# Optimization experiments

Hardware: AMD Instinct MI355X
Metric: run time of the kernel (lower is better)

Reference implementation:

```python
import jax, jax.numpy as jnp
import numpy as np
import math

D_K = 64
ROUNDS = 4
BUCKET_LEN = 64


def _l2norm(x, axis):
    n = jnp.sqrt(jnp.sum(x * x, axis=axis, keepdims=True))
    return x / jnp.maximum(n, 1e-12)


def _look_back(x):
    # x: (B, n_buckets, bucket_len, ...) -> (B, n_buckets, 2*bucket_len, ...)
    # each bucket is concatenated with the previous bucket (wrapping at 0)
    shift = jnp.concatenate([x[:, -1:], x[:, :-1]], axis=1)
    return jnp.concatenate([shift, x], axis=2)


def _lsh_hash(query, rand_matrix):
    # returns position-tagged hashes: bucket_id * L + position, shape (B, L, R)
    B, L, D = query.shape
    qn = _l2norm(query, -1)
    rm = _l2norm(rand_matrix, 1)  # normalize over d_k dim, as in torch code
    xR = jnp.einsum('bld,bdrn->blrn', qn, rm)
    h = jnp.argmax(jnp.concatenate([xR, -xR], axis=-1), axis=-1).astype(jnp.int32)
    return h * L + jnp.arange(L, dtype=jnp.int32)[None, :, None]


def _attend(query, value, hash_indice, original_indice, sorted_hashes):
    B, L, D = query.shape
    nb = L // BUCKET_LEN
    R = ROUNDS
    # gather queries into hash-sorted order, per round: (B, L, D, R)
    rq = jnp.take_along_axis(query[:, :, :, None], hash_indice[:, :, None, :], axis=1)
    rq = rq.reshape(B, nb, BUCKET_LEN, D, R)
    lk = _l2norm(_look_back(rq), -2)  # keys = normalized lookback queries (shared QK)
    qk = jnp.einsum('bnijk,bnljk->bnilk', rq, lk) / math.sqrt(D_K)  # (B,nb,bl,2bl,R)
    # mask cross-bucket pairs
    sh = (sorted_hashes // L).reshape(B, nb, BUCKET_LEN, R)
    qk = jnp.where(sh[..., None, :] != _look_back(sh)[..., None, :, :], -1e9, qk)
    # mask self-attention (causal=False so no causal mask)
    qi = hash_indice.reshape(B, nb, BUCKET_LEN, R).astype(jnp.int32)
    ki = _look_back(qi)
    qk = jnp.where(qi[..., None, :] == ki[..., None, :, :], -1e5, qk)
    qk = qk.reshape(B, L, 2 * BUCKET_LEN, R)
    lse = jax.scipy.special.logsumexp(qk, axis=2)  # (B, L, R)
    p = jnp.exp(qk - lse[:, :, None, :]).reshape(B, nb, BUCKET_LEN, 2 * BUCKET_LEN, R)
    # gather values into sorted order and apply lookback attention
    rv = jnp.take_along_axis(value[:, :, :, None], hash_indice[:, :, None, :], axis=1)
    rv = rv.reshape(B, nb, BUCKET_LEN, D, R)
    att = jnp.einsum('bnijl,bnjkl->bnikl', p, _look_back(rv)).reshape(B, L, D, R)
    # scatter back to original order
    att = jnp.take_along_axis(att, original_indice[:, :, None, :], axis=1)
    lse = jnp.take_along_axis(lse, original_indice, axis=1)
    # NOTE: faithful to source, softmax over dim=1 (sequence dim)
    w = jax.nn.softmax(lse, axis=1)  # (B, L, R)
    return jnp.einsum('blir,blr->bli', att, w)  # (B, L, D)


def setup_inputs() -> dict:
    key = jax.random.key(0)
    k1, k2, k3 = jax.random.split(key, 3)
    B, L, D = 16, 8192, D_K
    n_buckets = L // BUCKET_LEN
    return {
        'query': jax.random.normal(k1, (B, L, D), jnp.float32),
        'value': jax.random.normal(k2, (B, L, D), jnp.float32),
        'rand_matrix': jax.random.normal(k3, (B, D, ROUNDS, n_buckets // 2), jnp.float32),
    }


def reference(query, value, rand_matrix):
    hashes = _lsh_hash(query, rand_matrix)          # (B, L, R) int32
    hash_indice = jnp.argsort(hashes, axis=1)       # sort positions by hash
    sorted_hashes = jnp.take_along_axis(hashes, hash_indice, axis=1)
    original_indice = jnp.argsort(hash_indice, axis=1)  # inverse permutation
    return _attend(query, value, hash_indice.astype(jnp.int32),
                   original_indice.astype(jnp.int32), sorted_hashes)
```

## Files before the change

kernel.cpp:

```cpp
#include <hip/hip_runtime.h>
#include <math.h>

#define B_   16
#define L_   8192
#define D_   64
#define R_   4
#define NB_  128
#define NH_  64

typedef float v2f __attribute__((ext_vector_type(2)));

__device__ __forceinline__ float dpp_xor1(float x) {
    return __int_as_float(__builtin_amdgcn_mov_dpp(__float_as_int(x), 0xB1, 0xf, 0xf, true));
}
__device__ __forceinline__ float dpp_xor2(float x) {
    return __int_as_float(__builtin_amdgcn_mov_dpp(__float_as_int(x), 0x4E, 0xf, 0xf, true));
}
__device__ __forceinline__ float quad_bcast0(float x) {
    return __int_as_float(__builtin_amdgcn_mov_dpp(__float_as_int(x), 0x00, 0xf, 0xf, true));
}
__device__ __forceinline__ float quad_bcast1(float x) {
    return __int_as_float(__builtin_amdgcn_mov_dpp(__float_as_int(x), 0x55, 0xf, 0xf, true));
}
__device__ __forceinline__ float quad_bcast2(float x) {
    return __int_as_float(__builtin_amdgcn_mov_dpp(__float_as_int(x), 0xAA, 0xf, 0xf, true));
}
__device__ __forceinline__ float quad_bcast3(float x) {
    return __int_as_float(__builtin_amdgcn_mov_dpp(__float_as_int(x), 0xFF, 0xf, 0xf, true));
}

__global__ __launch_bounds__(64) void k_rmnorm(const float* __restrict__ rm, double* __restrict__ rmn) {
    int b = blockIdx.x >> 2, r = blockIdx.x & 3;
    int n = threadIdx.x;
    float v[D_];
    double ss = 0.0;
    #pragma unroll
    for (int d = 0; d < D_; ++d) {
        float f = rm[((size_t)(b * D_ + d) * R_ + r) * NH_ + n];
        v[d] = f;
        ss += (double)f * (double)f;
    }
    double nrm = sqrt(ss); if (nrm < 1e-12) nrm = 1e-12;
    double inv = 1.0 / nrm;
    double* o = rmn + ((size_t)(b * R_ + r) * NH_ + n) * D_;
    #pragma unroll
    for (int d = 0; d < D_; ++d) o[d] = (double)v[d] * inv;
}

__global__ __launch_bounds__(256) void k_hash(const float* __restrict__ q, const double* __restrict__ rmn,
                                              float* __restrict__ rn, int* __restrict__ h) {
    __shared__ float rms[NH_ * D_];
    int b = blockIdx.z, r = blockIdx.y;
    int l = blockIdx.x * 256 + threadIdx.x;
    const double* src = rmn + (size_t)(b * R_ + r) * NH_ * D_;
    for (int i = threadIdx.x; i < NH_ * D_; i += 256) rms[i] = (float)src[i];
    const float* qp = q + ((size_t)b * L_ + l) * D_;
    v2f qv2[D_ / 2];
    double ss = 0.0;
    #pragma unroll
    for (int d = 0; d < D_; d += 4) {
        float4 f = *(const float4*)(qp + d);
        qv2[d >> 1]       = (v2f){f.x, f.y};
        qv2[(d >> 1) + 1] = (v2f){f.z, f.w};
        ss += (double)f.x * f.x + (double)f.y * f.y + (double)f.z * f.z + (double)f.w * f.w;
    }
    __syncthreads();
    float best = -1.0e30f, second = -1.0e30f; int bi = 0;
    for (int n = 0; n < NH_; ++n) {
        const float* kp = &rms[n * D_];
        v2f a0 = (v2f){0.f, 0.f}, a1 = a0;
        #pragma unroll
        for (int d = 0; d < D_; d += 4) {
            float4 kk = *(const float4*)(kp + d);
            a0 = __builtin_elementwise_fma(qv2[d >> 1],       (v2f){kk.x, kk.y}, a0);
            a1 = __builtin_elementwise_fma(qv2[(d >> 1) + 1], (v2f){kk.z, kk.w}, a1);
        }
        float s = (a0.x + a0.y) + (a1.x + a1.y);
        if (s > best)       { second = best; best = s; bi = n; }
        else if (s > second)  second = s;
        float ns = -s;
        if (ns > best)      { second = best; best = ns; bi = n + NH_; }
        else if (ns > second) second = ns;
    }
    float qn = (float)sqrt(ss);
    if (best - second < 1.2e-5f * qn + 1.0e-7f) {
        double bestd = -1.0e300; bi = 0;
        for (int n = 0; n < NH_; ++n) {
            const double* kp = src + n * D_;
            double a0 = 0, a1 = 0, a2 = 0, a3 = 0;
            #pragma unroll
            for (int d = 0; d < D_; d += 4) {
                a0 = fma((double)qv2[d >> 1].x,       kp[d],     a0);
                a1 = fma((double)qv2[d >> 1].y,       kp[d + 1], a1);
                a2 = fma((double)qv2[(d >> 1) + 1].x, kp[d + 2], a2);
                a3 = fma((double)qv2[(d >> 1) + 1].y, kp[d + 3], a3);
            }
            double s = (a0 + a1) + (a2 + a3);
            if (s > bestd)  { bestd = s;  bi = n; }
            if (-s > bestd) { bestd = -s; bi = n + NH_; }
        }
    }
    h[(size_t)(b * R_ + r) * L_ + l] = bi;
    if (r == 0) {
        double nrm = sqrt(ss); if (nrm < 1e-12) nrm = 1e-12;
        rn[(size_t)b * L_ + l] = (float)(1.0 / nrm);
    }
}

__global__ __launch_bounds__(256) void k_sort(const int* __restrict__ h, const float* __restrict__ rn,
                                              int* __restrict__ iv, int2* __restrict__ rec) {
    __shared__ unsigned int cnt[NB_ * 257];
    __shared__ unsigned int wsum[4];
    int br = blockIdx.x;
    const int* hh = h + (size_t)br * L_;
    const float* rnb = rn + (size_t)(br >> 2) * L_;
    int t = threadIdx.x;
    for (int i = t; i < NB_ * 257; i += 256) cnt[i] = 0;
    __syncthreads();
    int base = t * 32;
    for (int i = 0; i < 32; ++i) { int bk = hh[base + i]; cnt[bk * 257 + t]++; }
    __syncthreads();
    int fb = t * 128;
    unsigned int local = 0;
    for (int i = 0; i < 128; ++i) { unsigned g = fb + i; local += cnt[g + (g >> 8)]; }
    unsigned int v = local;
    #pragma unroll
    for (int off = 1; off < 64; off <<= 1) {
        unsigned int u = __shfl_up(v, off);
        if ((t & 63) >= off) v += u;
    }
    if ((t & 63) == 63) wsum[t >> 6] = v;
    __syncthreads();
    unsigned int wbase = 0;
    for (int w = 0; w < (t >> 6); ++w) wbase += wsum[w];
    unsigned int run = wbase + v - local;
    for (int i = 0; i < 128; ++i) {
        unsigned g = fb + i;
        unsigned int c0 = cnt[g + (g >> 8)];
        cnt[g + (g >> 8)] = run; run += c0;
    }
    __syncthreads();
    int* ivp = iv + (size_t)br * L_;
    int2* rp = rec + (size_t)br * L_;
    for (int i = 0; i < 32; ++i) {
        int l = base + i; int bk = hh[l];
        unsigned int pos = cnt[bk * 257 + t]++;
        ivp[l] = (int)pos;
        rp[pos] = make_int2(l | (bk << 16), __float_as_int(rnb[l]));
    }
}

__global__ __launch_bounds__(128, 2) void k_flash(const float* __restrict__ q, const float* __restrict__ val,
                                                  const int2* __restrict__ rec, float* __restrict__ lse,
                                                  const float* __restrict__ gm, const float* __restrict__ gs,
                                                  float* __restrict__ out, float* __restrict__ contrib,
                                                  int r_fixed, int omode) {
    __shared__ float kt[2][16 * 80];
    __shared__ float vt[2][16 * 80];
    __shared__ int2  krc[2][16];
    int w   = threadIdx.x >> 6;
    int tid = threadIdx.x & 63;
    int c = blockIdx.x * 2 + w, b = blockIdx.z;
    int r = (r_fixed < 0) ? (int)blockIdx.y : r_fixed;
    size_t sbase = (size_t)(b * R_ + r) * L_;
    const int2* recs = rec + sbase;
    const float* qb = q   + (size_t)b * L_ * D_;
    const float* vb = val + (size_t)b * L_ * D_;
    int loadv = (omode != 2);
    int h = tid & 3;
    int posq = c * 64 + (tid >> 2) * 4;
    int2 rown = recs[posq + h];
    int own_w0 = rown.x;
    int own_bk = own_w0 & 0xFFFF0000;
    float m_own = 0.125f / __int_as_float(rown.y);
    int minbk = __builtin_amdgcn_readfirstlane(recs[c * 64].x) & 0xFFFF0000;
    int maxbk = __builtin_amdgcn_readfirstlane(recs[c * 64 + 63].x) & 0xFFFF0000;
    int mls[4];
    #pragma unroll
    for (int qq = 0; qq < 4; ++qq) mls[qq] = recs[posq + qq].x & 0xFFFF;
    int ownpos = posq + h;
    v2f qv2[4][8];
    #pragma unroll
    for (int qq = 0; qq < 4; ++qq) {
        const float* qp = qb + (size_t)mls[qq] * D_ + h * 16;
        #pragma unroll
        for (int i = 0; i < 16; i += 4) {
            float4 f = *(const float4*)(qp + i);
            qv2[qq][i >> 1]       = (v2f){f.x, f.y};
            qv2[qq][(i >> 1) + 1] = (v2f){f.z, f.w};
        }
    }
    float ps[4] = {0.0f, 0.0f, 0.0f, 0.0f};
    v2f acc2[4][8];
    #pragma unroll
    for (int qq = 0; qq < 4; ++qq)
        #pragma unroll
        for (int i = 0; i < 8; ++i) acc2[qq][i] = (v2f){0.0f, 0.0f};

    #pragma unroll 1
    for (int s = 0; s < 8; ++s) {
        int ck = ((c + NB_ - 1 + (s >> 2)) & (NB_ - 1)) * 64 + (s & 3) * 16;
        int sfir = __builtin_amdgcn_readfirstlane(recs[ck].x) & 0xFFFF0000;
        int slas = __builtin_amdgcn_readfirstlane(recs[ck + 15].x) & 0xFFFF0000;
        if (slas < minbk || sfir > maxbk) continue;
        {
            int rw = tid >> 2, cc = tid & 3;
            int kl = recs[ck + rw].x & 0xFFFF;
            const float* kp = qb + (size_t)kl * D_ + cc * 16;
            float* kd = &kt[w][rw * 80 + cc * 20];
            #pragma unroll
            for (int i = 0; i < 16; i += 4) *(float4*)(kd + i) = *(const float4*)(kp + i);
            if (loadv) {
                const float* vp = vb + (size_t)kl * D_ + cc * 16;
                float* vd = &vt[w][rw * 80 + cc * 20];
                #pragma unroll
                for (int i = 0; i < 16; i += 4) *(float4*)(vd + i) = *(const float4*)(vp + i);
            }
            if (tid < 16) krc[w][tid] = recs[ck + tid];
        }
        #pragma unroll
        for (int j = 0; j < 16; ++j) {
            int2 kv = krc[w][j];
            int bkj = __builtin_amdgcn_readfirstlane(kv.x) & 0xFFFF0000;
            if (bkj < minbk || bkj > maxbk) continue;
            const float* kpj = &kt[w][j * 80 + h * 20];
            v2f a0 = (v2f){0.f, 0.f}, a1 = a0, a2 = a0, a3 = a0;
            #pragma unroll
            for (int i = 0; i < 16; i += 4) {
                float4 kk = *(const float4*)(kpj + i);
                v2f kA = (v2f){kk.x, kk.y}, kB = (v2f){kk.z, kk.w};
                int i2 = i >> 1;
                a0 = __builtin_elementwise_fma(qv2[0][i2], kA, a0);
                a0 = __builtin_elementwise_fma(qv2[0][i2 + 1], kB, a0);
                a1 = __builtin_elementwise_fma(qv2[1][i2], kA, a1);
                a1 = __builtin_elementwise_fma(qv2[1][i2 + 1], kB, a1);
                a2 = __builtin_elementwise_fma(qv2[2][i2], kA, a2);
                a2 = __builtin_elementwise_fma(qv2[2][i2 + 1], kB, a2);
                a3 = __builtin_elementwise_fma(qv2[3][i2], kA, a3);
                a3 = __builtin_elementwise_fma(qv2[3][i2 + 1], kB, a3);
            }
            float p0 = a0.x + a0.y, p1 = a1.x + a1.y, p2 = a2.x + a2.y, p3 = a3.x + a3.y;
            bool b0 = (h & 1), b1 = (h & 2) != 0;
            float u0 = b0 ? p1 : p0;
            float t0 = b0 ? p0 : p1;
            u0 += dpp_xor1(t0);
            float u2 = b0 ? p3 : p2;
            float t2 = b0 ? p2 : p3;
            u2 += dpp_xor1(t2);
            float dot = b1 ? u2 : u0;
            float t3 = b1 ? u0 : u2;
            dot += dpp_xor2(t3);
            float skr = __int_as_float(kv.y) * 0.125f;
            float sc = dot * skr;
            sc = (own_bk == (kv.x & 0xFFFF0000)) ? sc : -1.0e9f;
            if (own_w0 == kv.x) sc = -1.0e5f;
            float p = __expf(sc - m_own);
            ps[j & 3] += p;
            if (loadv) {
                v2f P0 = (v2f){quad_bcast0(p), quad_bcast0(p)};
                v2f P1 = (v2f){quad_bcast1(p), quad_bcast1(p)};
                v2f P2 = (v2f){quad_bcast2(p), quad_bcast2(p)};
                v2f P3 = (v2f){quad_bcast3(p), quad_bcast3(p)};
                const float* vpj = &vt[w][j * 80 + h * 20];
                float4 vv0 = *(const float4*)(vpj + 0);
                float4 vv1 = *(const float4*)(vpj + 4);
                float4 vv2 = *(const float4*)(vpj + 8);
                float4 vv3 = *(const float4*)(vpj + 12);
                v2f vAa = (v2f){vv0.x, vv0.y}, vAb = (v2f){vv0.z, vv0.w};
                v2f vAc = (v2f){vv1.x, vv1.y}, vAd = (v2f){vv1.z, vv1.w};
                v2f vAe = (v2f){vv2.x, vv2.y}, vAf = (v2f){vv2.z, vv2.w};
                v2f vAg = (v2f){vv3.x, vv3.y}, vAh = (v2f){vv3.z, vv3.w};
                acc2[0][0] = __builtin_elementwise_fma(P0, vAa, acc2[0][0]);
                acc2[0][1] = __builtin_elementwise_fma(P0, vAb, acc2[0][1]);
                acc2[0][2] = __builtin_elementwise_fma(P0, vAc, acc2[0][2]);
                acc2[0][3] = __builtin_elementwise_fma(P0, vAd, acc2[0][3]);
                acc2[0][4] = __builtin_elementwise_fma(P0, vAe, acc2[0][4]);
                acc2[0][5] = __builtin_elementwise_fma(P0, vAf, acc2[0][5]);
                acc2[0][6] = __builtin_elementwise_fma(P0, vAg, acc2[0][6]);
                acc2[0][7] = __builtin_elementwise_fma(P0, vAh, acc2[0][7]);
                acc2[1][0] = __builtin_elementwise_fma(P1, vAa, acc2[1][0]);
                acc2[1][1] = __builtin_elementwise_fma(P1, vAb, acc2[1][1]);
                acc2[1][2] = __builtin_elementwise_fma(P1, vAc, acc2[1][2]);
                acc2[1][3] = __builtin_elementwise_fma(P1, vAd, acc2[1][3]);
                acc2[1][4] = __builtin_elementwise_fma(P1, vAe, acc2[1][4]);
                acc2[1][5] = __builtin_elementwise_fma(P1, vAf, acc2[1][5]);
                acc2[1][6] = __builtin_elementwise_fma(P1, vAg, acc2[1][6]);
                acc2[1][7] = __builtin_elementwise_fma(P1, vAh, acc2[1][7]);
                acc2[2][0] = __builtin_elementwise_fma(P2, vAa, acc2[2][0]);
                acc2[2][1] = __builtin_elementwise_fma(P2, vAb, acc2[2][1]);
                acc2[2][2] = __builtin_elementwise_fma(P2, vAc, acc2[2][2]);
                acc2[2][3] = __builtin_elementwise_fma(P2, vAd, acc2[2][3]);
                acc2[2][4] = __builtin_elementwise_fma(P2, vAe, acc2[2][4]);
                acc2[2][5] = __builtin_elementwise_fma(P2, vAf, acc2[2][5]);
                acc2[2][6] = __builtin_elementwise_fma(P2, vAg, acc2[2][6]);
                acc2[2][7] = __builtin_elementwise_fma(P2, vAh, acc2[2][7]);
                acc2[3][0] = __builtin_elementwise_fma(P3, vAa, acc2[3][0]);
                acc2[3][1] = __builtin_elementwise_fma(P3, vAb, acc2[3][1]);
                acc2[3][2] = __builtin_elementwise_fma(P3, vAc, acc2[3][2]);
                acc2[3][3] = __builtin_elementwise_fma(P3, vAd, acc2[3][3]);
                acc2[3][4] = __builtin_elementwise_fma(P3, vAe, acc2[3][4]);
                acc2[3][5] = __builtin_elementwise_fma(P3, vAf, acc2[3][5]);
                acc2[3][6] = __builtin_elementwise_fma(P3, vAg, acc2[3][6]);
                acc2[3][7] = __builtin_elementwise_fma(P3, vAh, acc2[3][7]);
            }
        }
    }
    float sum = (ps[0] + ps[1]) + (ps[2] + ps[3]);
    float lse_own, inv_own;
    if (sum > 0.0f) { lse_own = m_own + logf(sum); inv_own = 1.0f / sum; }
    else            { lse_own = -3.0e38f;          inv_own = 0.0f; }
    if (omode != 3) lse[sbase + ownpos] = lse_own;
    if (omode == 0 || omode == 1) {
        float ivs[4];
        ivs[0] = quad_bcast0(inv_own); ivs[1] = quad_bcast1(inv_own);
        ivs[2] = quad_bcast2(inv_own); ivs[3] = quad_bcast3(inv_own);
        float* cbase = contrib + ((omode == 0) ? (size_t)(b * R_ + r) * L_ : (size_t)b * L_) * D_;
        #pragma unroll
        for (int qq = 0; qq < 4; ++qq) {
            float* cp = cbase + (size_t)(posq + qq) * D_ + h * 16;
            #pragma unroll
            for (int i = 0; i < 16; i += 4) {
                int i2 = i >> 1;
                float4 o;
                o.x = acc2[qq][i2].x * ivs[qq];     o.y = acc2[qq][i2].y * ivs[qq];
                o.z = acc2[qq][i2 + 1].x * ivs[qq]; o.w = acc2[qq][i2 + 1].y * ivs[qq];
                *(float4*)(cp + i) = o;
            }
        }
    } else if (omode == 3) {
        int brr = b * R_ + r;
        float gmv = gm[brr], gsv = gs[brr];
        float ls4[4], iv4[4];
        ls4[0] = quad_bcast0(lse_own); ls4[1] = quad_bcast1(lse_own);
        ls4[2] = quad_bcast2(lse_own); ls4[3] = quad_bcast3(lse_own);
        iv4[0] = quad_bcast0(inv_own); iv4[1] = quad_bcast1(inv_own);
        iv4[2] = quad_bcast2(inv_own); iv4[3] = quad_bcast3(inv_own);
        #pragma unroll
        for (int qq = 0; qq < 4; ++qq) {
            float wq = __expf(ls4[qq] - gmv) * gsv * iv4[qq];
            float* op = out + ((size_t)b * L_ + mls[qq]) * D_ + h * 16;
            #pragma unroll
            for (int i = 0; i < 8; ++i) {
                unsafeAtomicAdd(op + 2 * i,     wq * acc2[qq][i].x);
                unsafeAtomicAdd(op + 2 * i + 1, wq * acc2[qq][i].y);
            }
        }
    }
}

__global__ __launch_bounds__(256) void k_wred(const float* __restrict__ lse, float* __restrict__ gm,
                                              float* __restrict__ gs, int r_w) {
    __shared__ float  sm[4];
    __shared__ double sd[4];
    int br = (r_w < 0) ? (int)blockIdx.x : ((int)blockIdx.x * R_ + r_w);
    const float* x = lse + (size_t)br * L_;
    int t = threadIdx.x;
    float mx = -3.0e38f;
    for (int i = t; i < L_; i += 256) mx = fmaxf(mx, x[i]);
    #pragma unroll
    for (int o = 32; o; o >>= 1) mx = fmaxf(mx, __shfl_down(mx, o));
    if ((t & 63) == 0) sm[t >> 6] = mx;
    __syncthreads();
    mx = fmaxf(fmaxf(sm[0], sm[1]), fmaxf(sm[2], sm[3]));
    double s = 0.0;
    for (int i = t; i < L_; i += 256) s += exp((double)x[i] - (double)mx);
    #pragma unroll
    for (int o = 32; o; o >>= 1) s += __shfl_down(s, o);
    if ((t & 63) == 0) sd[t >> 6] = s;
    __syncthreads();
    if (t == 0) { gm[br] = mx; gs[br] = (float)(1.0 / (sd[0] + sd[1] + sd[2] + sd[3])); }
}

__global__ __launch_bounds__(256) void k_comb_full(const float* __restrict__ contrib,
                                                   const int* __restrict__ iv,
                                                   const float* __restrict__ lse,
                                                   const float* __restrict__ gm,
                                                   const float* __restrict__ gs,
                                                   float* __restrict__ out) {
    int gid = blockIdx.x * 256 + threadIdx.x;
    int row = gid >> 2;
    int ch  = (gid & 3) * 16;
    int b = row >> 13, l = row & (L_ - 1);
    float s[16];
    #pragma unroll
    for (int i = 0; i < 16; ++i) s[i] = 0.0f;
    #pragma unroll
    for (int r = 0; r < R_; ++r) {
        int brr = b * R_ + r;
        int pos = iv[(size_t)brr * L_ + l];
        float w = expf(lse[(size_t)brr * L_ + pos] - gm[brr]) * gs[brr];
        const float* cp = contrib + ((size_t)brr * L_ + pos) * D_ + ch;
        #pragma unroll
        for (int i = 0; i < 16; i += 4) {
            float4 f = *(const float4*)(cp + i);
            s[i]   = fmaf(w, f.x, s[i]);   s[i+1] = fmaf(w, f.y, s[i+1]);
            s[i+2] = fmaf(w, f.z, s[i+2]); s[i+3] = fmaf(w, f.w, s[i+3]);
        }
    }
    float* op = out + (size_t)row * D_ + ch;
    #pragma unroll
    for (int i = 0; i < 16; i += 4) {
        float4 o; o.x = s[i]; o.y = s[i+1]; o.z = s[i+2]; o.w = s[i+3];
        *(float4*)(op + i) = o;
    }
}

__global__ __launch_bounds__(256) void k_comb_add(const float* __restrict__ contrib,
                                                  const int* __restrict__ iv,
                                                  const float* __restrict__ lse,
                                                  const float* __restrict__ gm,
                                                  const float* __restrict__ gs,
                                                  float* __restrict__ out, int r) {
    int gid = blockIdx.x * 256 + threadIdx.x;
    int row = gid >> 2;
    int ch  = (gid & 3) * 16;
    int b = row >> 13, l = row & (L_ - 1);
    int brr = b * R_ + r;
    int pos = iv[(size_t)brr * L_ + l];
    float w = expf(lse[(size_t)brr * L_ + pos] - gm[brr]) * gs[brr];
    const float* cp = contrib + ((size_t)b * L_ + pos) * D_ + ch;
    float* op = out + (size_t)row * D_ + ch;
    #pragma unroll
    for (int i = 0; i < 16; i += 4) {
        float4 f = *(const float4*)(cp + i);
        float4 o = *(const float4*)(op + i);
        o.x = fmaf(w, f.x, o.x); o.y = fmaf(w, f.y, o.y);
        o.z = fmaf(w, f.z, o.z); o.w = fmaf(w, f.w, o.w);
        *(float4*)(op + i) = o;
    }
}

#define OFF_RMN     0u
#define OFF_REC     0u
#define OFF_RN      4194304u
#define OFF_H       4718592u
#define OFF_LSE     6815744u
#define OFF_GM      8912896u
#define OFF_GS      8913152u
#define OFF_INV     8913408u
#define OFF_CONTRIB 11010560u
#define CONTRIB_FULL_BYTES  134217728ull
#define CONTRIB_SLICE_BYTES 33554432ull

extern "C" void kernel_launch(void* const* d_in, const int* in_sizes, int n_in,
                              void* d_out, int out_size, void* d_ws, size_t ws_size,
                              hipStream_t stream) {
    const float* q  = (const float*)d_in[0];
    const float* v  = (const float*)d_in[1];
    const float* rm = (const float*)d_in[2];
    float* out = (float*)d_out;
    char* ws = (char*)d_ws;
    double* rmn = (double*)(ws + OFF_RMN);
    int2*   rec = (int2*)(ws + OFF_REC);
    float*  rn  = (float*)(ws + OFF_RN);
    int*    h   = (int*)(ws + OFF_H);
    float*  lse = (float*)(ws + OFF_LSE);
    float*  gm  = (float*)(ws + OFF_GM);
    float*  gs  = (float*)(ws + OFF_GS);
    int*    iv  = (int*)(ws + OFF_INV);
    float*  contrib = (float*)(ws + OFF_CONTRIB);

    int tierA = (ws_size >= (size_t)OFF_CONTRIB + CONTRIB_FULL_BYTES) ? 1 : 0;
    int tierB = (!tierA && ws_size >= (size_t)OFF_CONTRIB + CONTRIB_SLICE_BYTES) ? 1 : 0;

    hipLaunchKernelGGL(k_rmnorm, dim3(B_ * R_), dim3(64), 0, stream, rm, rmn);
    hipLaunchKernelGGL(k_hash, dim3(L_ / 256, R_, B_), dim3(256), 0, stream, q, rmn, rn, h);
    hipLaunchKernelGGL(k_sort, dim3(B_ * R_), dim3(256), 0, stream, h, rn, iv, rec);

    if (tierA) {
        hipLaunchKernelGGL(k_flash, dim3(NB_ / 2, R_, B_), dim3(128), 0, stream, q, v, rec,
                           lse, gm, gs, out, contrib, -1, 0);
        hipLaunchKernelGGL(k_wred, dim3(B_ * R_), dim3(256), 0, stream, lse, gm, gs, -1);
        hipLaunchKernelGGL(k_comb_full, dim3(B_ * L_ * 4 / 256), dim3(256), 0, stream,
                           contrib, iv, lse, gm, gs, out);
    } else if (tierB) {
        hipMemsetAsync(d_out, 0, (size_t)B_ * L_ * D_ * sizeof(float), stream);
        for (int r = 0; r < R_; ++r) {
            hipLaunchKernelGGL(k_flash, dim3(NB_ / 2, 1, B_), dim3(128), 0, stream, q, v, rec,
                               lse, gm, gs, out, contrib, r, 1);
            hipLaunchKernelGGL(k_wred, dim3(B_), dim3(256), 0, stream, lse, gm, gs, r);
            hipLaunchKernelGGL(k_comb_add, dim3(B_ * L_ * 4 / 256), dim3(256), 0, stream,
                               contrib, iv, lse, gm, gs, out, r);
        }
    } else {
        hipMemsetAsync(d_out, 0, (size_t)B_ * L_ * D_ * sizeof(float), stream);
        hipLaunchKernelGGL(k_flash, dim3(NB_ / 2, R_, B_), dim3(128), 0, stream, q, v, rec,
                           lse, gm, gs, out, contrib, -1, 2);
        hipLaunchKernelGGL(k_wred, dim3(B_ * R_), dim3(256), 0, stream, lse, gm, gs, -1);
        hipLaunchKernelGGL(k_flash, dim3(NB_ / 2, R_, B_), dim3(128), 0, stream, q, v, rec,
                           lse, gm, gs, out, contrib, -1, 3);
    }
}
```

Before: 530.1 us.

## Hash two positions per thread, prestore float rotations, skip out-of-range key loads

The hash kernel now computes two sequence positions per thread, so each shared-memory read of the rotation matrix feeds twice as many FMAs, and the grid is halved to match. The normalisation kernel also writes a float copy of the rotations, so the hash kernel loads it with float4 instead of converting doubles. In the flash kernel, key and value rows whose bucket falls outside the query tile's range are no longer loaded into shared memory. The float copy shares its workspace offset with the inverse-permutation buffer, which is safe only if that buffer is written after hashing. Doubling per-thread work also raises register pressure.

After: 560.4 us. 5.7% more time.

```diff
diff --git a/kernel.cpp b/kernel.cpp
--- a/kernel.cpp
+++ b/kernel.cpp
@@ -29,7 +29,8 @@
     return __int_as_float(__builtin_amdgcn_mov_dpp(__float_as_int(x), 0xFF, 0xf, 0xf, true));
 }
 
-__global__ __launch_bounds__(64) void k_rmnorm(const float* __restrict__ rm, double* __restrict__ rmn) {
+__global__ __launch_bounds__(64) void k_rmnorm(const float* __restrict__ rm, double* __restrict__ rmn,
+                                               float* __restrict__ rmf) {
     int b = blockIdx.x >> 2, r = blockIdx.x & 3;
     int n = threadIdx.x;
     float v[D_];
@@ -42,68 +43,115 @@
     }
     double nrm = sqrt(ss); if (nrm < 1e-12) nrm = 1e-12;
     double inv = 1.0 / nrm;
-    double* o = rmn + ((size_t)(b * R_ + r) * NH_ + n) * D_;
-    #pragma unroll
-    for (int d = 0; d < D_; ++d) o[d] = (double)v[d] * inv;
-}
-
-__global__ __launch_bounds__(256) void k_hash(const float* __restrict__ q, const double* __restrict__ rmn,
-                                              float* __restrict__ rn, int* __restrict__ h) {
+    double* o  = rmn + ((size_t)(b * R_ + r) * NH_ + n) * D_;
+    float*  of = rmf + ((size_t)(b * R_ + r) * NH_ + n) * D_;
+    #pragma unroll
+    for (int d = 0; d < D_; ++d) {
+        double dv = (double)v[d] * inv;
+        o[d] = dv;
+        of[d] = (float)dv;
+    }
+}
+
+__global__ __launch_bounds__(256, 2) void k_hash(const float* __restrict__ q, const double* __restrict__ rmn,
+                                                 const float* __restrict__ rmf,
+                                                 float* __restrict__ rn, int* __restrict__ h) {
     __shared__ float rms[NH_ * D_];
     int b = blockIdx.z, r = blockIdx.y;
-    int l = blockIdx.x * 256 + threadIdx.x;
+    int t = threadIdx.x;
+    int l0 = blockIdx.x * 512 + t;
+    int l1 = l0 + 256;
     const double* src = rmn + (size_t)(b * R_ + r) * NH_ * D_;
-    for (int i = threadIdx.x; i < NH_ * D_; i += 256) rms[i] = (float)src[i];
-    const float* qp = q + ((size_t)b * L_ + l) * D_;
-    v2f qv2[D_ / 2];
-    double ss = 0.0;
+    const float* srcf = rmf + (size_t)(b * R_ + r) * NH_ * D_;
+    for (int i = t * 4; i < NH_ * D_; i += 1024)
+        *(float4*)&rms[i] = *(const float4*)&srcf[i];
+    const float* qp0 = q + ((size_t)b * L_ + l0) * D_;
+    const float* qp1 = q + ((size_t)b * L_ + l1) * D_;
+    v2f qa[D_ / 2], qb[D_ / 2];
+    double ssa = 0.0, ssb = 0.0;
     #pragma unroll
     for (int d = 0; d < D_; d += 4) {
-        float4 f = *(const float4*)(qp + d);
-        qv2[d >> 1]       = (v2f){f.x, f.y};
-        qv2[(d >> 1) + 1] = (v2f){f.z, f.w};
-        ss += (double)f.x * f.x + (double)f.y * f.y + (double)f.z * f.z + (double)f.w * f.w;
-    }
-    __syncthreads();
-    float best = -1.0e30f, second = -1.0e30f; int bi = 0;
+        float4 f = *(const float4*)(qp0 + d);
+        qa[d >> 1]       = (v2f){f.x, f.y};
+        qa[(d >> 1) + 1] = (v2f){f.z, f.w};
+        ssa += (double)f.x * f.x + (double)f.y * f.y + (double)f.z * f.z + (double)f.w * f.w;
+        float4 g = *(const float4*)(qp1 + d);
+        qb[d >> 1]       = (v2f){g.x, g.y};
+        qb[(d >> 1) + 1] = (v2f){g.z, g.w};
+        ssb += (double)g.x * g.x + (double)g.y * g.y + (double)g.z * g.z + (double)g.w * g.w;
+    }
+    __syncthreads();
+    float besta = -1.0e30f, seconda = -1.0e30f; int bia = 0;
+    float bestb = -1.0e30f, secondb = -1.0e30f; int bib = 0;
     for (int n = 0; n < NH_; ++n) {
         const float* kp = &rms[n * D_];
-        v2f a0 = (v2f){0.f, 0.f}, a1 = a0;
+        v2f a0 = (v2f){0.f, 0.f}, a1 = a0, c0 = a0, c1 = a0;
         #pragma unroll
         for (int d = 0; d < D_; d += 4) {
             float4 kk = *(const float4*)(kp + d);
-            a0 = __builtin_elementwise_fma(qv2[d >> 1],       (v2f){kk.x, kk.y}, a0);
-            a1 = __builtin_elementwise_fma(qv2[(d >> 1) + 1], (v2f){kk.z, kk.w}, a1);
-        }
-        float s = (a0.x + a0.y) + (a1.x + a1.y);
-        if (s > best)       { second = best; best = s; bi = n; }
-        else if (s > second)  second = s;
-        float ns = -s;
-        if (ns > best)      { second = best; best = ns; bi = n + NH_; }
-        else if (ns > second) second = ns;
-    }
-    float qn = (float)sqrt(ss);
-    if (best - second < 1.2e-5f * qn + 1.0e-7f) {
-        double bestd = -1.0e300; bi = 0;
+            v2f kA = (v2f){kk.x, kk.y}, kB = (v2f){kk.z, kk.w};
+            int i2 = d >> 1;
+            a0 = __builtin_elementwise_fma(qa[i2],     kA, a0);
+            a1 = __builtin_elementwise_fma(qa[i2 + 1], kB, a1);
+            c0 = __builtin_elementwise_fma(qb[i2],     kA, c0);
+            c1 = __builtin_elementwise_fma(qb[i2 + 1], kB, c1);
+        }
+        float sa = (a0.x + a0.y) + (a1.x + a1.y);
+        if (sa > besta)        { seconda = besta; besta = sa; bia = n; }
+        else if (sa > seconda)   seconda = sa;
+        float nsa = -sa;
+        if (nsa > besta)       { seconda = besta; besta = nsa; bia = n + NH_; }
+        else if (nsa > seconda)  seconda = nsa;
+        float sb = (c0.x + c0.y) + (c1.x + c1.y);
+        if (sb > bestb)        { secondb = bestb; bestb = sb; bib = n; }
+        else if (sb > secondb)   secondb = sb;
+        float nsb = -sb;
+        if (nsb > bestb)       { secondb = bestb; bestb = nsb; bib = n + NH_; }
+        else if (nsb > secondb)  secondb = nsb;
+    }
+    float qna = (float)sqrt(ssa);
+    if (besta - seconda < 1.2e-5f * qna + 1.0e-7f) {
+        double bestd = -1.0e300; bia = 0;
         for (int n = 0; n < NH_; ++n) {
             const double* kp = src + n * D_;
             double a0 = 0, a1 = 0, a2 = 0, a3 = 0;
             #pragma unroll
             for (int d = 0; d < D_; d += 4) {
-                a0 = fma((double)qv2[d >> 1].x,       kp[d],     a0);
-                a1 = fma((double)qv2[d >> 1].y,       kp[d + 1], a1);
-                a2 = fma((double)qv2[(d >> 1) + 1].x, kp[d + 2], a2);
-                a3 = fma((double)qv2[(d >> 1) + 1].y, kp[d + 3], a3);
+                a0 = fma((double)qa[d >> 1].x,       kp[d],     a0);
+                a1 = fma((double)qa[d >> 1].y,       kp[d + 1], a1);
+                a2 = fma((double)qa[(d >> 1) + 1].x, kp[d + 2], a2);
+                a3 = fma((double)qa[(d >> 1) + 1].y, kp[d + 3], a3);
             }
             double s = (a0 + a1) + (a2 + a3);
-            if (s > bestd)  { bestd = s;  bi = n; }
-            if (-s > bestd) { bestd = -s; bi = n + NH_; }
-        }
-    }
-    h[(size_t)(b * R_ + r) * L_ + l] = bi;
+            if (s > bestd)  { bestd = s;  bia = n; }
+            if (-s > bestd) { bestd = -s; bia = n + NH_; }
+        }
+    }
+    float qnb = (float)sqrt(ssb);
+    if (bestb - secondb < 1.2e-5f * qnb + 1.0e-7f) {
+        double bestd = -1.0e300; bib = 0;
+        for (int n = 0; n < NH_; ++n) {
+            const double* kp = src + n * D_;
+            double a0 = 0, a1 = 0, a2 = 0, a3 = 0;
+            #pragma unroll
+            for (int d = 0; d < D_; d += 4) {
+                a0 = fma((double)qb[d >> 1].x,       kp[d],     a0);
+                a1 = fma((double)qb[d >> 1].y,       kp[d + 1], a1);
+                a2 = fma((double)qb[(d >> 1) + 1].x, kp[d + 2], a2);
+                a3 = fma((double)qb[(d >> 1) + 1].y, kp[d + 3], a3);
+            }
+            double s = (a0 + a1) + (a2 + a3);
+            if (s > bestd)  { bestd = s;  bib = n; }
+            if (-s > bestd) { bestd = -s; bib = n + NH_; }
+        }
+    }
+    h[(size_t)(b * R_ + r) * L_ + l0] = bia;
+    h[(size_t)(b * R_ + r) * L_ + l1] = bib;
     if (r == 0) {
-        double nrm = sqrt(ss); if (nrm < 1e-12) nrm = 1e-12;
-        rn[(size_t)b * L_ + l] = (float)(1.0 / nrm);
+        double na = sqrt(ssa); if (na < 1e-12) na = 1e-12;
+        rn[(size_t)b * L_ + l0] = (float)(1.0 / na);
+        double nb = sqrt(ssb); if (nb < 1e-12) nb = 1e-12;
+        rn[(size_t)b * L_ + l1] = (float)(1.0 / nb);
     }
 }
 
@@ -205,16 +253,20 @@
         if (slas < minbk || sfir > maxbk) continue;
         {
             int rw = tid >> 2, cc = tid & 3;
-            int kl = recs[ck + rw].x & 0xFFFF;
-            const float* kp = qb + (size_t)kl * D_ + cc * 16;
-            float* kd = &kt[w][rw * 80 + cc * 20];
-            #pragma unroll
-            for (int i = 0; i < 16; i += 4) *(float4*)(kd + i) = *(const float4*)(kp + i);
-            if (loadv) {
-                const float* vp = vb + (size_t)kl * D_ + cc * 16;
-                float* vd = &vt[w][rw * 80 + cc * 20];
+            int rrec = recs[ck + rw].x;
+            int rbk = rrec & 0xFFFF0000;
+            if (rbk >= minbk && rbk <= maxbk) {
+                int kl = rrec & 0xFFFF;
+                const float* kp = qb + (size_t)kl * D_ + cc * 16;
+                float* kd = &kt[w][rw * 80 + cc * 20];
                 #pragma unroll
-                for (int i = 0; i < 16; i += 4) *(float4*)(vd + i) = *(const float4*)(vp + i);
+                for (int i = 0; i < 16; i += 4) *(float4*)(kd + i) = *(const float4*)(kp + i);
+                if (loadv) {
+                    const float* vp = vb + (size_t)kl * D_ + cc * 16;
+                    float* vd = &vt[w][rw * 80 + cc * 20];
+                    #pragma unroll
+                    for (int i = 0; i < 16; i += 4) *(float4*)(vd + i) = *(const float4*)(vp + i);
+                }
             }
             if (tid < 16) krc[w][tid] = recs[ck + tid];
         }
@@ -438,6 +490,7 @@
 #define OFF_GM      8912896u
 #define OFF_GS      8913152u
 #define OFF_INV     8913408u
+#define OFF_RMF     8913408u
 #define OFF_CONTRIB 11010560u
 #define CONTRIB_FULL_BYTES  134217728ull
 #define CONTRIB_SLICE_BYTES 33554432ull
@@ -458,13 +511,14 @@
     float*  gm  = (float*)(ws + OFF_GM);
     float*  gs  = (float*)(ws + OFF_GS);
     int*    iv  = (int*)(ws + OFF_INV);
+    float*  rmf = (float*)(ws + OFF_RMF);
     float*  contrib = (float*)(ws + OFF_CONTRIB);
 
     int tierA = (ws_size >= (size_t)OFF_CONTRIB + CONTRIB_FULL_BYTES) ? 1 : 0;
     int tierB = (!tierA && ws_size >= (size_t)OFF_CONTRIB + CONTRIB_SLICE_BYTES) ? 1 : 0;
 
-    hipLaunchKernelGGL(k_rmnorm, dim3(B_ * R_), dim3(64), 0, stream, rm, rmn);
-    hipLaunchKernelGGL(k_hash, dim3(L_ / 256, R_, B_), dim3(256), 0, stream, q, rmn, rn, h);
+    hipLaunchKernelGGL(k_rmnorm, dim3(B_ * R_), dim3(64), 0, stream, rm, rmn, rmf);
+    hipLaunchKernelGGL(k_hash, dim3(L_ / 512, R_, B_), dim3(256), 0, stream, q, rmn, rmf, rn, h);
     hipLaunchKernelGGL(k_sort, dim3(B_ * R_), dim3(256), 0, stream, h, rn, iv, rec);
 
     if (tierA) {
```
